# Kernel tuning notes

Measured on AMD Instinct MI355X. Metric: run time of the kernel, lower is better.

The kernel has to match this reference:

```python
import jax, jax.numpy as jnp
import numpy as np

NUM_TAGS = 32            # init arg
N = NUM_TAGS + 2         # internal num_tags (start/end appended)
START = N - 2
END = N - 1
B = 1024
T = 1024
NEG = -6969.0            # module's 'minus infinity' constant


def setup_inputs() -> dict:
    key = jax.random.key(0)
    k1, k2 = jax.random.split(key)
    features = jax.random.normal(k1, (B, T, N), dtype=jnp.float32)
    # learned parameter: transition matrix [N, N]
    transitions = jax.random.normal(k2, (N, N), dtype=jnp.float32)
    return {"features": features, "transitions": transitions}


def _viterbi(features, transitions):
    # features: [B, T, N]; transitions: [N, N]
    Bn, Tn, Nn = features.shape
    init = jnp.full((Bn, Nn), NEG, dtype=features.dtype).at[:, START].set(0.0)

    def step(scores, feat):
        # score[b, j, k] = scores[b, k] + feat[b, j] + transitions[j, k]
        sc = scores[:, None, :] + feat[:, :, None] + transitions[None, :, :]
        return jnp.max(sc, axis=-1), jnp.argmax(sc, axis=-1)

    feats_t = jnp.swapaxes(features, 0, 1)            # [T, B, N]
    scores, paths = jax.lax.scan(step, init, feats_t)  # paths: [T, B, N] int

    scores = scores + transitions[END]                # add transition to end tag
    best = jnp.max(scores, axis=-1)                   # [B]
    idx = jnp.argmax(scores, axis=-1)                 # [B]

    # backtrack through backpointers, from t = T-1 down to 0
    def back(i, path):
        ni = jnp.take_along_axis(path, i[:, None], axis=1)[:, 0]
        return ni, ni

    _, tags = jax.lax.scan(back, idx, paths, reverse=True)  # tags: [T, B]
    best_path = jnp.concatenate([tags.T, idx[:, None]], axis=1)  # [B, T+1]
    return best, best_path


def reference(features, transitions):
    return _viterbi(features, transitions)
```

## Files before the change

### kernel.cpp

```cpp
#include <hip/hip_runtime.h>
#include <stdint.h>

#define BB 1024
#define TT 1024
#define NN 34
#define NEGV -6969.0f

__device__ __forceinline__ float rdlane_f(float v, int l) {
    return __int_as_float(__builtin_amdgcn_readlane(__float_as_int(v), l));
}

__global__ __launch_bounds__(64) void viterbi_wave(
        const float* __restrict__ feat,
        const float* __restrict__ trans,
        float* __restrict__ out)
{
    __shared__ unsigned char bp[TT * NN];
    __shared__ unsigned char Fm[16 * NN];

    const int lane = threadIdx.x;
    const int bg   = blockIdx.x;
    const int jc   = (lane < NN) ? lane : (NN - 1);

    float tr[NN];
#pragma unroll
    for (int k = 0; k < NN; ++k) tr[k] = trans[jc * NN + k];
    const float trE = trans[33 * NN + jc];

    const float* fp = feat + (size_t)bg * TT * NN + jc;
    float fr0 = fp[0 * NN], fr1 = fp[1 * NN], fr2 = fp[2 * NN], fr3 = fp[3 * NN];

    float sk[NN];
#pragma unroll
    for (int k = 0; k < NN; ++k) sk[k] = (k == 32) ? 0.0f : NEGV;

    float m = NEGV;
    int tbase = 0;

    auto vstep = [&](float f) {
        float vv[NN];
#pragma unroll
        for (int k = 0; k < NN; ++k) vv[k] = (sk[k] + f) + tr[k];

        float t0[17];
#pragma unroll
        for (int k = 0; k < 17; ++k) t0[k] = fmaxf(vv[2 * k], vv[2 * k + 1]);
        float t1[8];
#pragma unroll
        for (int k = 0; k < 8; ++k) t1[k] = fmaxf(t0[2 * k], t0[2 * k + 1]);
        float t2a = fmaxf(fmaxf(t1[0], t1[1]), fmaxf(t1[2], t1[3]));
        float t2b = fmaxf(fmaxf(t1[4], t1[5]), fmaxf(t1[6], t1[7]));
        float mx  = fmaxf(fmaxf(t2a, t2b), t0[16]);

        int am0 = 127, am1 = 127, am2 = 127, am3 = 127;
#pragma unroll
        for (int k = NN - 1; k >= 0; --k) {
            bool e = (vv[k] == mx);
            if ((k & 3) == 0) am0 = e ? k : am0;
            else if ((k & 3) == 1) am1 = e ? k : am1;
            else if ((k & 3) == 2) am2 = e ? k : am2;
            else am3 = e ? k : am3;
        }
        int am = min(min(am0, am1), min(am2, am3));

        if (lane < NN) bp[tbase + lane] = (unsigned char)am;
        tbase += NN;

#pragma unroll
        for (int k = 0; k < NN; ++k) sk[k] = rdlane_f(mx, k);
        m = mx;
    };

    for (int n = 0; n < 255; ++n) {
        { float f = fr0; fr0 = fp[4 * NN]; vstep(f); }
        { float f = fr1; fr1 = fp[5 * NN]; vstep(f); }
        { float f = fr2; fr2 = fp[6 * NN]; vstep(f); }
        { float f = fr3; fr3 = fp[7 * NN]; vstep(f); }
        fp += 4 * NN;
    }
    vstep(fr0); vstep(fr1); vstep(fr2); vstep(fr3);

    float fs = m + trE;
    float bm = rdlane_f(fs, 0);
    int bi = 0;
#pragma unroll
    for (int k = 1; k < NN; ++k) {
        float v = rdlane_f(fs, k);
        bool g = (v > bm);
        bm = g ? v : bm;
        bi = g ? k : bi;
    }
    if (lane == 0) out[bg] = bm;

    int cc[9], xx[9], mm[9], cb[9];
#pragma unroll
    for (int r = 0; r < 9; ++r) {
        int job = 64 * r + lane;
        if (job > 543) job = 543;
        cc[r] = job / 34;
        xx[r] = job - 34 * cc[r];
        mm[r] = xx[r];
        cb[r] = cc[r] * (64 * NN);
    }
    for (int i = 63; i >= 0; --i) {
        int ib = i * NN;
#pragma unroll
        for (int r = 0; r < 9; ++r) mm[r] = bp[cb[r] + ib + mm[r]];
    }
#pragma unroll
    for (int r = 0; r < 9; ++r) Fm[cc[r] * NN + xx[r]] = (unsigned char)mm[r];

    int e = bi;
    int myeb = (lane == 15) ? e : 0;
#pragma unroll
    for (int c2 = 15; c2 >= 1; --c2) {
        e = Fm[c2 * NN + e];
        myeb = (lane == c2 - 1) ? e : myeb;
    }

    float* po = out + BB + (size_t)bg * (TT + 1);
    if (lane < 16) {
        int mm2 = myeb;
        int base = lane * (64 * NN);
        for (int i = 63; i >= 0; --i) {
            mm2 = bp[base + i * NN + mm2];
            po[lane * 64 + i] = (float)mm2;
        }
    }
    if (lane == 16) po[TT] = (float)bi;
}

extern "C" void kernel_launch(void* const* d_in, const int* in_sizes, int n_in,
                              void* d_out, int out_size, void* d_ws, size_t ws_size,
                              hipStream_t stream) {
    const float* feat  = (const float*)d_in[0];
    const float* trans = (const float*)d_in[1];
    float* out = (float*)d_out;

    viterbi_wave<<<BB, 64, 0, stream>>>(feat, trans, out);
}
```

Measured before the change: 674.2 us.

## Use packed f32 adds and broadcast scores through LDS instead of readlane

The per-step score computation now uses v_pk_add_f32 on paired values, halving the add instruction count. The 34 v_readlane broadcasts of the new max scores are replaced by one LDS store per lane followed by 17 vector LDS reads of float pairs, which moves the cross-lane exchange off the scalar path. Occupancy is pinned via launch_bounds(64,1). The trade-off is LDS round-trip latency on the serial recurrence, with no explicit barrier (relying on single-wave execution).

```diff
diff --git a/kernel.cpp b/kernel.cpp
--- a/kernel.cpp
+++ b/kernel.cpp
@@ -6,68 +6,88 @@
 #define NN 34
 #define NEGV -6969.0f
 
+typedef float v2f __attribute__((ext_vector_type(2)));
+
+__device__ __forceinline__ v2f pk_add(v2f a, v2f b) {
+    v2f d;
+    asm("v_pk_add_f32 %0, %1, %2" : "=v"(d) : "v"(a), "v"(b));
+    return d;
+}
+
 __device__ __forceinline__ float rdlane_f(float v, int l) {
     return __int_as_float(__builtin_amdgcn_readlane(__float_as_int(v), l));
 }
 
-__global__ __launch_bounds__(64) void viterbi_wave(
+__global__ __launch_bounds__(64, 1) void viterbi_wave(
         const float* __restrict__ feat,
         const float* __restrict__ trans,
         float* __restrict__ out)
 {
     __shared__ unsigned char bp[TT * NN];
+    __shared__ __align__(16) float sc[64];
     __shared__ unsigned char Fm[16 * NN];
 
     const int lane = threadIdx.x;
     const int bg   = blockIdx.x;
     const int jc   = (lane < NN) ? lane : (NN - 1);
 
-    float tr[NN];
+    v2f tr2[17];
 #pragma unroll
-    for (int k = 0; k < NN; ++k) tr[k] = trans[jc * NN + k];
+    for (int p = 0; p < 17; ++p) {
+        tr2[p].x = trans[jc * NN + 2 * p];
+        tr2[p].y = trans[jc * NN + 2 * p + 1];
+    }
     const float trE = trans[33 * NN + jc];
 
     const float* fp = feat + (size_t)bg * TT * NN + jc;
     float fr0 = fp[0 * NN], fr1 = fp[1 * NN], fr2 = fp[2 * NN], fr3 = fp[3 * NN];
 
-    float sk[NN];
+    v2f sk2[17];
 #pragma unroll
-    for (int k = 0; k < NN; ++k) sk[k] = (k == 32) ? 0.0f : NEGV;
+    for (int p = 0; p < 17; ++p) { sk2[p].x = NEGV; sk2[p].y = NEGV; }
+    sk2[16].x = 0.0f;
 
     float m = NEGV;
     int tbase = 0;
 
     auto vstep = [&](float f) {
-        float vv[NN];
+        v2f f2; f2.x = f; f2.y = f;
+        v2f q[17];
 #pragma unroll
-        for (int k = 0; k < NN; ++k) vv[k] = (sk[k] + f) + tr[k];
+        for (int p = 0; p < 17; ++p) q[p] = pk_add(pk_add(sk2[p], f2), tr2[p]);
 
-        float t0[17];
+        float pm[17];
 #pragma unroll
-        for (int k = 0; k < 17; ++k) t0[k] = fmaxf(vv[2 * k], vv[2 * k + 1]);
-        float t1[8];
+        for (int p = 0; p < 17; ++p) pm[p] = fmaxf(q[p].x, q[p].y);
+        float u0 = fmaxf(fmaxf(pm[0], pm[1]),   fmaxf(pm[2], pm[3]));
+        float u1 = fmaxf(fmaxf(pm[4], pm[5]),   fmaxf(pm[6], pm[7]));
+        float u2 = fmaxf(fmaxf(pm[8], pm[9]),   fmaxf(pm[10], pm[11]));
+        float u3 = fmaxf(fmaxf(pm[12], pm[13]), fmaxf(pm[14], pm[15]));
+        float mx = fmaxf(fmaxf(fmaxf(u0, u1), fmaxf(u2, u3)), pm[16]);
+
+        sc[lane] = mx;
 #pragma unroll
-        for (int k = 0; k < 8; ++k) t1[k] = fmaxf(t0[2 * k], t0[2 * k + 1]);
-        float t2a = fmaxf(fmaxf(t1[0], t1[1]), fmaxf(t1[2], t1[3]));
-        float t2b = fmaxf(fmaxf(t1[4], t1[5]), fmaxf(t1[6], t1[7]));
-        float mx  = fmaxf(fmaxf(t2a, t2b), t0[16]);
+        for (int p = 0; p < 17; ++p) sk2[p] = *(const v2f*)&sc[2 * p];
 
         int am0 = 127, am1 = 127, am2 = 127, am3 = 127;
 #pragma unroll
-        for (int k = NN - 1; k >= 0; --k) {
-            bool e = (vv[k] == mx);
-            if ((k & 3) == 0) am0 = e ? k : am0;
-            else if ((k & 3) == 1) am1 = e ? k : am1;
-            else if ((k & 3) == 2) am2 = e ? k : am2;
-            else am3 = e ? k : am3;
+        for (int p = 16; p >= 0; --p) {
+            int k0 = 2 * p, k1 = 2 * p + 1;
+            bool e1 = (q[p].y == mx);
+            if ((k1 & 3) == 0) am0 = e1 ? k1 : am0;
+            else if ((k1 & 3) == 1) am1 = e1 ? k1 : am1;
+            else if ((k1 & 3) == 2) am2 = e1 ? k1 : am2;
+            else am3 = e1 ? k1 : am3;
+            bool e0 = (q[p].x == mx);
+            if ((k0 & 3) == 0) am0 = e0 ? k0 : am0;
+            else if ((k0 & 3) == 1) am1 = e0 ? k0 : am1;
+            else if ((k0 & 3) == 2) am2 = e0 ? k0 : am2;
+            else am3 = e0 ? k0 : am3;
         }
         int am = min(min(am0, am1), min(am2, am3));
 
         if (lane < NN) bp[tbase + lane] = (unsigned char)am;
         tbase += NN;
-
-#pragma unroll
-        for (int k = 0; k < NN; ++k) sk[k] = rdlane_f(mx, k);
         m = mx;
     };
 
```

Result: faster. 604.8 us (-10.3%).
